# Optimization experiments

Hardware: AMD Instinct MI355X
Metric: run time of the kernel (lower is better)

## Reference

```python
import jax, jax.numpy as jnp
import numpy as np

N = 100000  # nodes
E = 1600000  # edges (before self-loops)
F_IN, F_HID, F_OUT = 64, 128, 64


def setup_inputs() -> dict:
    key = jax.random.key(0)
    ks = jax.random.split(key, 8)
    x = jax.random.normal(ks[0], (N, F_IN), dtype=jnp.float32)
    edge_index = jax.random.randint(ks[1], (2, E), 0, N, dtype=jnp.int64)
    # Glorot-ish init for weights, zero bias (PyG GCNConv default)
    W1 = jax.random.normal(ks[2], (F_IN, F_HID), dtype=jnp.float32) / np.sqrt(F_IN)
    W2 = jax.random.normal(ks[3], (F_HID, F_HID), dtype=jnp.float32) / np.sqrt(F_HID)
    W3 = jax.random.normal(ks[4], (F_HID, F_OUT), dtype=jnp.float32) / np.sqrt(F_HID)
    b1 = jnp.zeros((F_HID,), dtype=jnp.float32)
    b2 = jnp.zeros((F_HID,), dtype=jnp.float32)
    b3 = jnp.zeros((F_OUT,), dtype=jnp.float32)
    return {"x": x, "edge_index": edge_index, "W1": W1, "b1": b1,
            "W2": W2, "b2": b2, "W3": W3, "b3": b3}


def _gcn_norm(edge_index, num_nodes):
    """Add self-loops and compute symmetric D^-1/2 A D^-1/2 edge norms."""
    loop = jnp.arange(num_nodes, dtype=edge_index.dtype)
    src = jnp.concatenate([edge_index[0], loop])  # [E+N]
    dst = jnp.concatenate([edge_index[1], loop])  # [E+N]
    deg = jax.ops.segment_sum(jnp.ones_like(src, dtype=jnp.float32), dst,
                              num_segments=num_nodes)
    dinv = jnp.where(deg > 0, jax.lax.rsqrt(deg), 0.0)
    norm = dinv[src] * dinv[dst]  # [E+N]
    return src, dst, norm


def _gcn_conv(h, src, dst, norm, W, b, num_nodes):
    hw = h @ W                                   # [N, out] dense transform
    msg = hw[src] * norm[:, None]                # gather + edge scale
    out = jax.ops.segment_sum(msg, dst, num_segments=num_nodes)  # scatter-add
    return out + b


def reference(x, edge_index, W1, b1, W2, b2, W3, b3):
    src, dst, norm = _gcn_norm(edge_index, N)
    h = jax.nn.relu(_gcn_conv(x, src, dst, norm, W1, b1, N))
    h = jax.nn.relu(_gcn_conv(h, src, dst, norm, W2, b2, N))
    return _gcn_conv(h, src, dst, norm, W3, b3, N)
```

## Files before the change

kernel.cpp:

```cpp
#include <hip/hip_runtime.h>
#include <hip/hip_bf16.h>
#include <hip/hip_fp16.h>


typedef _Float16 h8 __attribute__((ext_vector_type(8)));
typedef float f4 __attribute__((ext_vector_type(4)));

constexpr int BSHIFT = 7;
constexpr int BNODES = 1 << BSHIFT;
constexpr int PB     = 256;
constexpr int CAP    = 4096;

__device__ inline void load8h(const _Float16* p, float* f) {
    h8 v = *(const h8*)p;
#pragma unroll
    for (int j = 0; j < 8; j++) f[j] = (float)v[j];
}

__device__ inline void store8h(_Float16* p, const float* f) {
    h8 v;
#pragma unroll
    for (int j = 0; j < 8; j++) v[j] = (_Float16)f[j];
    *(h8*)p = v;
}

__device__ inline void store4h(_Float16* p, float4 v) {
    _Float16 t[4] = {(_Float16)v.x, (_Float16)v.y, (_Float16)v.z, (_Float16)v.w};
    *(uint2*)p = *(uint2*)t;
}

__global__ __launch_bounds__(256) void phist_k(const int* __restrict__ dst,
                                               int* __restrict__ hist,
                                               int E, int nbuck, int chunk) {
    __shared__ int h[1024];
    for (int i = threadIdx.x; i < nbuck; i += 256) h[i] = 0;
    __syncthreads();
    int beg = blockIdx.x * chunk;
    int end = min(E, beg + chunk);
    for (int e = beg + threadIdx.x; e < end; e += 256)
        atomicAdd(&h[dst[e] >> BSHIFT], 1);
    __syncthreads();
    for (int i = threadIdx.x; i < nbuck; i += 256)
        hist[(long)blockIdx.x * nbuck + i] = h[i];
}

__global__ __launch_bounds__(256) void scan_blocks_k(const int* __restrict__ in,
                                                     int* __restrict__ excl,
                                                     int* __restrict__ bsums, int n) {
    __shared__ int s[256];
    int tid = threadIdx.x;
    int i = blockIdx.x * 256 + tid;
    int v = (i < n) ? in[i] : 0;
    s[tid] = v;
    __syncthreads();
    for (int off = 1; off < 256; off <<= 1) {
        int t = (tid >= off) ? s[tid - off] : 0;
        __syncthreads();
        s[tid] += t;
        __syncthreads();
    }
    if (i < n) excl[i] = s[tid] - v;
    if (tid == 255) bsums[blockIdx.x] = s[255];
}

__global__ __launch_bounds__(1024) void mid_k(int* __restrict__ bsums, int nb,
                                              const int* __restrict__ hist,
                                              int* __restrict__ bbase,
                                              int nbuck, int E) {
    __shared__ int s[1024];
    int tid = threadIdx.x;
    int v = 0;
    if (blockIdx.x == 0) {
        v = (tid < nb) ? bsums[tid] : 0;
    } else {
        if (tid < nbuck) {
            int t0 = 0, t1 = 0, t2 = 0, t3 = 0;
            for (int j = 0; j < PB; j += 4) {
                t0 += hist[(long)(j + 0) * nbuck + tid];
                t1 += hist[(long)(j + 1) * nbuck + tid];
                t2 += hist[(long)(j + 2) * nbuck + tid];
                t3 += hist[(long)(j + 3) * nbuck + tid];
            }
            v = (t0 + t1) + (t2 + t3);
        }
    }
    s[tid] = v;
    __syncthreads();
    for (int off = 1; off < 1024; off <<= 1) {
        int t = (tid >= off) ? s[tid - off] : 0;
        __syncthreads();
        s[tid] += t;
        __syncthreads();
    }
    if (blockIdx.x == 0) {
        if (tid < nb) bsums[tid] = s[tid] - v;
    } else {
        if (tid < nbuck) bbase[tid] = s[tid] - v;
        if (tid == 0) bbase[nbuck] = E;
    }
}

__global__ __launch_bounds__(256) void part2_k(const int* __restrict__ src,
                                               const int* __restrict__ dst,
                                               const int* __restrict__ offs,
                                               const int* __restrict__ bsums,
                                               unsigned* __restrict__ ebuf,
                                               int E, int nbuck, int chunk) {
    __shared__ int cur[1024];
    for (int i = threadIdx.x; i < nbuck; i += 256) {
        long flat = (long)blockIdx.x * nbuck + i;
        cur[i] = offs[flat] + bsums[flat >> 8];
    }
    __syncthreads();
    int beg = blockIdx.x * chunk;
    int end = min(E, beg + chunk);
    for (int e = beg + threadIdx.x; e < end; e += 256) {
        int d = dst[e];
        int b = d >> BSHIFT;
        int pos = atomicAdd(&cur[b], 1);
        ebuf[pos] = ((unsigned)(d & (BNODES - 1)) << 25) | (unsigned)src[e];
    }
}

__global__ __launch_bounds__(256) void finalize_k(const unsigned* __restrict__ ebuf,
                                                  const int* __restrict__ hist,
                                                  const int* __restrict__ offs,
                                                  const int* __restrict__ bsums,
                                                  const int* __restrict__ bbase,
                                                  int nbuck,
                                                  int* __restrict__ rowst,
                                                  int* __restrict__ rowend,
                                                  float* __restrict__ dinv,
                                                  int* __restrict__ col,
                                                  const float* __restrict__ x,
                                                  _Float16* __restrict__ msgX, int N) {
    __shared__ unsigned se[CAP];
    __shared__ int cj[PB], sj[PB], sb[PB];
    __shared__ int cnt_s[BNODES], scan_s[BNODES], cur_s[BNODES];
    __shared__ float di_s[BNODES];

    int b = blockIdx.x, tid = threadIdx.x;
    int node0 = b << BSHIFT;
    int nn = min(BNODES, N - node0);
    int beg = bbase[b];

    if (tid < PB) {
        long flat = (long)tid * nbuck + b;
        cj[tid] = hist[flat];
        sj[tid] = offs[flat] + bsums[flat >> 8];
    }
    if (tid < BNODES) cnt_s[tid] = 0;
    __syncthreads();

    if (tid < PB) sb[tid] = cj[tid];
    __syncthreads();
    for (int off = 1; off < PB; off <<= 1) {
        int t = 0;
        if (tid < PB && tid >= off) t = sb[tid - off];
        __syncthreads();
        if (tid < PB) sb[tid] += t;
        __syncthreads();
    }
    int m = sb[PB - 1];
    __syncthreads();

    {
        int j = tid;
        int base = sb[j] - cj[j], c = cj[j], s0 = sj[j];
        for (int k = 0; k < c; k++) {
            unsigned e = ebuf[s0 + k];
            int idx = base + k;
            if (idx < CAP) se[idx] = e;
            else atomicAdd(&cnt_s[e >> 25], 1);
        }
    }
    __syncthreads();

    int mcap = m < CAP ? m : CAP;
    for (int i = tid; i < mcap; i += 256) atomicAdd(&cnt_s[se[i] >> 25], 1);
    __syncthreads();

    int v = (tid < BNODES) ? cnt_s[tid] : 0;
    if (tid < BNODES) scan_s[tid] = v;
    __syncthreads();
    for (int off = 1; off < BNODES; off <<= 1) {
        int t = 0;
        if (tid < BNODES && tid >= off) t = scan_s[tid - off];
        __syncthreads();
        if (tid < BNODES) scan_s[tid] += t;
        __syncthreads();
    }
    if (tid < nn) {
        int ex = scan_s[tid] - v;
        int st = beg + ex;
        rowst[node0 + tid] = st;
        rowend[node0 + tid] = st + v;
        float di = rsqrtf((float)v + 1.0f);
        dinv[node0 + tid] = di;
        di_s[tid] = di;
        cur_s[tid] = ex;
    }
    __syncthreads();

    for (int i = tid; i < mcap; i += 256) {
        unsigned e = se[i];
        int p = atomicAdd(&cur_s[e >> 25], 1);
        col[beg + p] = (int)(e & 0x1FFFFFFu);
    }
    if (m > CAP) {
        int j = tid;
        int base = sb[j] - cj[j], c = cj[j], s0 = sj[j];
        for (int k = 0; k < c; k++) {
            int idx = base + k;
            if (idx >= CAP) {
                unsigned e = ebuf[s0 + k];
                int p = atomicAdd(&cur_s[e >> 25], 1);
                col[beg + p] = (int)(e & 0x1FFFFFFu);
            }
        }
    }

    for (int t = tid; t < nn * 16; t += 256) {
        int nl = t >> 4, q = t & 15;
        int node = node0 + nl;
        float4 vx = *(const float4*)(x + (long)node * 64 + q * 4);
        float di = di_s[nl];
        vx.x *= di; vx.y *= di; vx.z *= di; vx.w *= di;
        store4h(msgX + (long)node * 64 + q * 4, vx);
    }
}

template <int K, int FOUT, bool BIAS, bool RELU, bool DINV_OUT>
__global__ __launch_bounds__(256) void fag_k(const _Float16* __restrict__ msg,
                                             const int* __restrict__ rowst,
                                             const int* __restrict__ rowend,
                                             const int* __restrict__ col,
                                             const float* __restrict__ dinv,
                                             const _Float16* __restrict__ Wsw,
                                             const float* __restrict__ bias,
                                             _Float16* __restrict__ C, int n) {
    constexpr int NT = FOUT / 16, NC = K / 32;
    constexpr int LDK = K + 8;
    constexpr int LPN = K / 8;
    constexpr int NPB = 256 / LPN;
    __shared__ _Float16 As[64 * LDK];

    int tid = threadIdx.x;
    int row0 = blockIdx.x * 64;

#pragma unroll
    for (int pass = 0; pass < 64 / NPB; pass++) {
        int nl = pass * NPB + tid / LPN;
        int q = tid % LPN;
        int node = row0 + nl;
        float acc[8];
        if (node < n) {
            load8h(msg + (long)node * K + q * 8, acc);
            int beg = rowst[node], end = rowend[node];
            int e = beg;
            for (; e + 4 <= end; e += 4) {
                int s0 = col[e], s1 = col[e + 1], s2 = col[e + 2], s3 = col[e + 3];
                h8 v0 = *(const h8*)(msg + (long)s0 * K + q * 8);
                h8 v1 = *(const h8*)(msg + (long)s1 * K + q * 8);
                h8 v2 = *(const h8*)(msg + (long)s2 * K + q * 8);
                h8 v3 = *(const h8*)(msg + (long)s3 * K + q * 8);
#pragma unroll
                for (int j = 0; j < 8; j++)
                    acc[j] += ((float)v0[j] + (float)v1[j]) + ((float)v2[j] + (float)v3[j]);
            }
            for (; e < end; e++) {
                int s = col[e];
                h8 v = *(const h8*)(msg + (long)s * K + q * 8);
#pragma unroll
                for (int j = 0; j < 8; j++) acc[j] += (float)v[j];
            }
            float di = dinv[node];
#pragma unroll
            for (int j = 0; j < 8; j++) acc[j] *= di;
        } else {
#pragma unroll
            for (int j = 0; j < 8; j++) acc[j] = 0.f;
        }
        h8 o;
#pragma unroll
        for (int j = 0; j < 8; j++) o[j] = (_Float16)acc[j];
        *(h8*)(As + nl * LDK + q * 8) = o;
    }
    __syncthreads();

    int lane = tid & 63, wave = tid >> 6;
    int quad = lane >> 4, cl = lane & 15;
    int r0 = wave * 16;

    h8 a[NC];
#pragma unroll
    for (int c = 0; c < NC; c++)
        a[c] = *(const h8*)(As + (r0 + cl) * LDK + quad * 8 + c * 32);

    f4 acc2[NT];
#pragma unroll
    for (int t = 0; t < NT; t++) acc2[t] = (f4){0.f, 0.f, 0.f, 0.f};

    const h8* wv = (const h8*)Wsw;
#pragma unroll
    for (int c = 0; c < NC; c++) {
#pragma unroll
        for (int t = 0; t < NT; t++)
            acc2[t] = __builtin_amdgcn_mfma_f32_16x16x32_f16(
                a[c], wv[(c * NT + t) * 64 + lane], acc2[t], 0, 0, 0);
    }

#pragma unroll
    for (int t = 0; t < NT; t++) {
        int c0 = t * 16 + cl;
        float bb = BIAS ? bias[c0] : 0.f;
#pragma unroll
        for (int r = 0; r < 4; r++) {
            int row = row0 + r0 + quad * 4 + r;
            if (row >= n) continue;
            float v = acc2[t][r] + bb;
            if (RELU) v = fmaxf(v, 0.f);
            if (DINV_OUT) v *= dinv[row];
            C[(long)row * FOUT + c0] = (_Float16)v;
        }
    }
}

template <int F, bool BIAS, bool F16OUT>
__global__ __launch_bounds__(256) void agg_f16_k(const _Float16* __restrict__ msg,
                                                 const int* __restrict__ rowst,
                                                 const int* __restrict__ rowend,
                                                 const int* __restrict__ col,
                                                 const float* __restrict__ dinv,
                                                 const float* __restrict__ b,
                                                 void* __restrict__ out, int n) {
    constexpr int LPN = F / 8;
    constexpr int NPB = 256 / LPN;
    int node = blockIdx.x * NPB + threadIdx.x / LPN;
    int q = threadIdx.x % LPN;
    if (node >= n) return;

    float acc[8];
    load8h(msg + (long)node * F + q * 8, acc);

    int beg = rowst[node], end = rowend[node];
    int e = beg;
    for (; e + 8 <= end; e += 8) {
        h8 v[8];
#pragma unroll
        for (int u = 0; u < 8; u++)
            v[u] = *(const h8*)(msg + (long)col[e + u] * F + q * 8);
#pragma unroll
        for (int j = 0; j < 8; j++)
            acc[j] += (((float)v[0][j] + (float)v[1][j]) + ((float)v[2][j] + (float)v[3][j])) +
                      (((float)v[4][j] + (float)v[5][j]) + ((float)v[6][j] + (float)v[7][j]));
    }
    for (; e + 4 <= end; e += 4) {
        h8 v0 = *(const h8*)(msg + (long)col[e] * F + q * 8);
        h8 v1 = *(const h8*)(msg + (long)col[e + 1] * F + q * 8);
        h8 v2 = *(const h8*)(msg + (long)col[e + 2] * F + q * 8);
        h8 v3 = *(const h8*)(msg + (long)col[e + 3] * F + q * 8);
#pragma unroll
        for (int j = 0; j < 8; j++)
            acc[j] += ((float)v0[j] + (float)v1[j]) + ((float)v2[j] + (float)v3[j]);
    }
    for (; e < end; e++) {
        h8 v = *(const h8*)(msg + (long)col[e] * F + q * 8);
#pragma unroll
        for (int j = 0; j < 8; j++) acc[j] += (float)v[j];
    }

    float di = dinv[node];
    float o[8];
#pragma unroll
    for (int j = 0; j < 8; j++) o[j] = di * acc[j];
    if (BIAS) {
#pragma unroll
        for (int j = 0; j < 8; j++) o[j] += b[q * 8 + j];
    }
    if (F16OUT) {
        store8h((_Float16*)out + (long)node * F + q * 8, o);
    } else {
        float* dst = (float*)out + (long)node * F + q * 8;
        *(float4*)dst = make_float4(o[0], o[1], o[2], o[3]);
        *(float4*)(dst + 4) = make_float4(o[4], o[5], o[6], o[7]);
    }
}

template <int K, int FOUT>
__device__ inline void wfrag(const float* __restrict__ W,
                             _Float16* __restrict__ Wsw, int t) {
    constexpr int NT = FOUT / 16;
    int lane = t & 63;
    int tile = (t >> 6) % NT;
    int chunk = (t >> 6) / NT;
    int kbase = chunk * 32 + (lane >> 4) * 8;
    int nc = tile * 16 + (lane & 15);
    h8 v;
#pragma unroll
    for (int j = 0; j < 8; j++) v[j] = (_Float16)W[(kbase + j) * FOUT + nc];
    ((h8*)Wsw)[t] = v;
}

__global__ __launch_bounds__(256) void wprep3_k(const float* __restrict__ W1,
                                                const float* __restrict__ W2,
                                                const float* __restrict__ W3,
                                                _Float16* __restrict__ w1s,
                                                _Float16* __restrict__ w2s,
                                                _Float16* __restrict__ w3s) {
    int t = blockIdx.x * 256 + threadIdx.x;
    if (t < 1024) wfrag<64, 128>(W1, w1s, t);
    else if (t < 3072) wfrag<128, 128>(W2, w2s, t - 1024);
    else if (t < 4096) wfrag<128, 64>(W3, w3s, t - 3072);
}

__global__ __launch_bounds__(256) void dgemm_k(const _Float16* __restrict__ A,
                                               const _Float16* __restrict__ w2s,
                                               const _Float16* __restrict__ w3s,
                                               const float* __restrict__ b2,
                                               const float* __restrict__ dinv,
                                               _Float16* __restrict__ C, int n) {
    constexpr int LDK = 136;
    __shared__ _Float16 Hs[64 * LDK];

    int tid = threadIdx.x, lane = tid & 63, wave = tid >> 6;
    int quad = lane >> 4, cl = lane & 15;
    int row0 = blockIdx.x * 64, r0 = wave * 16;

    h8 a[4];
    const _Float16* arow = A + (long)(row0 + r0 + cl) * 128 + quad * 8;
#pragma unroll
    for (int c = 0; c < 4; c++) a[c] = *(const h8*)(arow + c * 32);

    f4 acc1[8];
#pragma unroll
    for (int t = 0; t < 8; t++) acc1[t] = (f4){0.f, 0.f, 0.f, 0.f};
    const h8* wv2 = (const h8*)w2s;
#pragma unroll
    for (int c = 0; c < 4; c++) {
#pragma unroll
        for (int t = 0; t < 8; t++)
            acc1[t] = __builtin_amdgcn_mfma_f32_16x16x32_f16(
                a[c], wv2[(c * 8 + t) * 64 + lane], acc1[t], 0, 0, 0);
    }

#pragma unroll
    for (int t = 0; t < 8; t++) {
        int c0 = t * 16 + cl;
        float bb = b2[c0];
#pragma unroll
        for (int r = 0; r < 4; r++) {
            float v = fmaxf(acc1[t][r] + bb, 0.f);
            Hs[(r0 + quad * 4 + r) * LDK + c0] = (_Float16)v;
        }
    }
    __builtin_amdgcn_s_waitcnt(0);

    h8 a2[4];
#pragma unroll
    for (int c = 0; c < 4; c++)
        a2[c] = *(const h8*)(Hs + (r0 + cl) * LDK + quad * 8 + c * 32);

    f4 acc2[4];
#pragma unroll
    for (int t = 0; t < 4; t++) acc2[t] = (f4){0.f, 0.f, 0.f, 0.f};
    const h8* wv3 = (const h8*)w3s;
#pragma unroll
    for (int c = 0; c < 4; c++) {
#pragma unroll
        for (int t = 0; t < 4; t++)
            acc2[t] = __builtin_amdgcn_mfma_f32_16x16x32_f16(
                a2[c], wv3[(c * 4 + t) * 64 + lane], acc2[t], 0, 0, 0);
    }

#pragma unroll
    for (int t = 0; t < 4; t++) {
        int c0 = t * 16 + cl;
#pragma unroll
        for (int r = 0; r < 4; r++) {
            int row = row0 + r0 + quad * 4 + r;
            if (row >= n) continue;
            float v = acc2[t][r] * dinv[row];
            C[(long)row * 64 + c0] = (_Float16)v;
        }
    }
}

extern "C" void kernel_launch(void* const* d_in, const int* in_sizes, int n_in,
                              void* d_out, int out_size, void* d_ws, size_t ws_size,
                              hipStream_t stream) {
    const float* x  = (const float*)d_in[0];
    const int*   ei = (const int*)d_in[1];
    const float* W1 = (const float*)d_in[2];
    const float* b1 = (const float*)d_in[3];
    const float* W2 = (const float*)d_in[4];
    const float* b2 = (const float*)d_in[5];
    const float* W3 = (const float*)d_in[6];
    const float* b3 = (const float*)d_in[7];
    float* out = (float*)d_out;

    const int N = in_sizes[0] / 64;
    const int E = in_sizes[1] / 2;
    const int* src = ei;
    const int* dst = ei + E;
    const int nbuck = (N + BNODES - 1) >> BSHIFT;
    const int chunk = (E + PB - 1) / PB;
    const int n2 = PB * nbuck;
    const int nb2 = (n2 + 255) / 256;

    int*   hist   = (int*)d_ws;
    int*   offs   = hist + n2;
    int*   bsums  = offs + n2;
    int*   bbase  = bsums + 1024;
    int*   rowst  = bbase + nbuck + 1;
    int*   rowend = rowst + N;
    float* dinv   = (float*)(rowend + N);
    int*   col    = (int*)(dinv + N);
    _Float16* w1s = (_Float16*)(col + E);
    _Float16* w2s = w1s + 64 * 128;
    _Float16* w3s = w2s + 128 * 128;
    float* P      = (float*)(w3s + 128 * 64);
    float* Q      = P + (long)N * 128;

    _Float16* msgX  = (_Float16*)P;
    unsigned* ebuf  = (unsigned*)Q;
    _Float16* msg1  = (_Float16*)Q;
    _Float16* aggH1 = (_Float16*)P;
    _Float16* msg3  = (_Float16*)Q;

    const int gb = (N + 63) / 64;

    wprep3_k<<<16, 256, 0, stream>>>(W1, W2, W3, w1s, w2s, w3s);

    phist_k<<<PB, 256, 0, stream>>>(dst, hist, E, nbuck, chunk);
    scan_blocks_k<<<nb2, 256, 0, stream>>>(hist, offs, bsums, n2);
    mid_k<<<2, 1024, 0, stream>>>(bsums, nb2, hist, bbase, nbuck, E);
    part2_k<<<PB, 256, 0, stream>>>(src, dst, offs, bsums, ebuf, E, nbuck, chunk);
    finalize_k<<<nbuck, 256, 0, stream>>>(ebuf, hist, offs, bsums, bbase, nbuck,
                                          rowst, rowend, dinv, col, x, msgX, N);

    fag_k<64, 128, true, true, true><<<gb, 256, 0, stream>>>(
        msgX, rowst, rowend, col, dinv, w1s, b1, msg1, N);

    agg_f16_k<128, false, true><<<(N + 15) / 16, 256, 0, stream>>>(
        msg1, rowst, rowend, col, dinv, nullptr, (void*)aggH1, N);

    dgemm_k<<<gb, 256, 0, stream>>>(aggH1, w2s, w3s, b2, dinv, msg3, N);

    agg_f16_k<64, true, false><<<(N + 31) / 32, 256, 0, stream>>>(
        msg3, rowst, rowend, col, dinv, b3, (void*)out, N);
}
```

Measured before the change: 383.6 us.

## Split aggregation kernels into feature slices for cache locality

The CSR aggregation kernels are changed so each block handles only one of eight feature slices (16 halfs for F=128, 8 halfs for F=64), with blockIdx low bits selecting the slice. Each gathered row segment is therefore narrower, so more rows of a slice fit in L2/MALL, which is meant to raise cache hit rates on the random neighbor gathers. In exchange, col indices and row pointers are re-read once per slice, and each gather becomes a 16-byte access per row, giving less coalescing per lane.

```diff
diff --git a/kernel.cpp b/kernel.cpp
--- a/kernel.cpp
+++ b/kernel.cpp
@@ -326,22 +326,26 @@
     }
 }
 
-template <int F, bool BIAS, bool F16OUT>
-__global__ __launch_bounds__(256) void agg_f16_k(const _Float16* __restrict__ msg,
-                                                 const int* __restrict__ rowst,
-                                                 const int* __restrict__ rowend,
-                                                 const int* __restrict__ col,
-                                                 const float* __restrict__ dinv,
-                                                 const float* __restrict__ b,
-                                                 void* __restrict__ out, int n) {
-    constexpr int LPN = F / 8;
-    constexpr int NPB = 256 / LPN;
-    int node = blockIdx.x * NPB + threadIdx.x / LPN;
-    int q = threadIdx.x % LPN;
+template <int F, int FS, bool BIAS, bool F16OUT>
+__global__ __launch_bounds__(256) void agg_slice_k(const _Float16* __restrict__ msg,
+                                                   const int* __restrict__ rowst,
+                                                   const int* __restrict__ rowend,
+                                                   const int* __restrict__ col,
+                                                   const float* __restrict__ dinv,
+                                                   const float* __restrict__ b,
+                                                   void* __restrict__ out, int n) {
+    constexpr int LPS = FS / 8;
+    constexpr int NPB = 256 / LPS;
+    int slice = blockIdx.x & 7;
+    int blk   = blockIdx.x >> 3;
+    int node  = blk * NPB + threadIdx.x / LPS;
+    int q     = threadIdx.x % LPS;
     if (node >= n) return;
+    int f0 = slice * FS + q * 8;
+    const _Float16* mp = msg + f0;
 
     float acc[8];
-    load8h(msg + (long)node * F + q * 8, acc);
+    load8h(mp + (long)node * F, acc);
 
     int beg = rowst[node], end = rowend[node];
     int e = beg;
@@ -349,23 +353,23 @@
         h8 v[8];
 #pragma unroll
         for (int u = 0; u < 8; u++)
-            v[u] = *(const h8*)(msg + (long)col[e + u] * F + q * 8);
+            v[u] = *(const h8*)(mp + (long)col[e + u] * F);
 #pragma unroll
         for (int j = 0; j < 8; j++)
             acc[j] += (((float)v[0][j] + (float)v[1][j]) + ((float)v[2][j] + (float)v[3][j])) +
                       (((float)v[4][j] + (float)v[5][j]) + ((float)v[6][j] + (float)v[7][j]));
     }
     for (; e + 4 <= end; e += 4) {
-        h8 v0 = *(const h8*)(msg + (long)col[e] * F + q * 8);
-        h8 v1 = *(const h8*)(msg + (long)col[e + 1] * F + q * 8);
-        h8 v2 = *(const h8*)(msg + (long)col[e + 2] * F + q * 8);
-        h8 v3 = *(const h8*)(msg + (long)col[e + 3] * F + q * 8);
+        h8 v0 = *(const h8*)(mp + (long)col[e] * F);
+        h8 v1 = *(const h8*)(mp + (long)col[e + 1] * F);
+        h8 v2 = *(const h8*)(mp + (long)col[e + 2] * F);
+        h8 v3 = *(const h8*)(mp + (long)col[e + 3] * F);
 #pragma unroll
         for (int j = 0; j < 8; j++)
             acc[j] += ((float)v0[j] + (float)v1[j]) + ((float)v2[j] + (float)v3[j]);
     }
     for (; e < end; e++) {
-        h8 v = *(const h8*)(msg + (long)col[e] * F + q * 8);
+        h8 v = *(const h8*)(mp + (long)col[e] * F);
 #pragma unroll
         for (int j = 0; j < 8; j++) acc[j] += (float)v[j];
     }
@@ -376,14 +380,14 @@
     for (int j = 0; j < 8; j++) o[j] = di * acc[j];
     if (BIAS) {
 #pragma unroll
-        for (int j = 0; j < 8; j++) o[j] += b[q * 8 + j];
+        for (int j = 0; j < 8; j++) o[j] += b[f0 + j];
     }
     if (F16OUT) {
-        store8h((_Float16*)out + (long)node * F + q * 8, o);
+        store8h((_Float16*)out + (long)node * F + f0, o);
     } else {
-        float* dst = (float*)out + (long)node * F + q * 8;
-        *(float4*)dst = make_float4(o[0], o[1], o[2], o[3]);
-        *(float4*)(dst + 4) = make_float4(o[4], o[5], o[6], o[7]);
+        float* d = (float*)out + (long)node * F + f0;
+        *(float4*)d = make_float4(o[0], o[1], o[2], o[3]);
+        *(float4*)(d + 4) = make_float4(o[4], o[5], o[6], o[7]);
     }
 }
 
@@ -542,11 +546,13 @@
     fag_k<64, 128, true, true, true><<<gb, 256, 0, stream>>>(
         msgX, rowst, rowend, col, dinv, w1s, b1, msg1, N);
 
-    agg_f16_k<128, false, true><<<(N + 15) / 16, 256, 0, stream>>>(
+    const int nb128 = (N + 127) / 128;
+    agg_slice_k<128, 16, false, true><<<8 * nb128, 256, 0, stream>>>(
         msg1, rowst, rowend, col, dinv, nullptr, (void*)aggH1, N);
 
     dgemm_k<<<gb, 256, 0, stream>>>(aggH1, w2s, w3s, b2, dinv, msg3, N);
 
-    agg_f16_k<64, true, false><<<(N + 31) / 32, 256, 0, stream>>>(
+    const int nb256 = (N + 255) / 256;
+    agg_slice_k<64, 8, true, false><<<8 * nb256, 256, 0, stream>>>(
         msg3, rowst, rowend, col, dinv, b3, (void*)out, N);
 }
```

Result: slower. 913.2 us (+138.1%).

## Slice layer-2 features into 16-column planes for cache-local aggregation

Applied to the files above, without the earlier changes.

The first fused aggregate-GEMM now writes its 128-wide output as eight 16-column slices, each stored contiguously over all nodes. A new aggregation kernel processes one slice per block, so the random gathers for a slice touch a working set of about 3.2 MB that can stay in cache. Each node's edges are split across four lanes and combined with shuffles. The following GEMM reads its A operand from this sliced layout. The cost is that every edge list is read eight times and the gathers are smaller (16 bytes each), in exchange for better cache hit rates.

```diff
diff --git a/kernel.cpp b/kernel.cpp
--- a/kernel.cpp
+++ b/kernel.cpp
@@ -230,7 +230,7 @@
     }
 }
 
-template <int K, int FOUT, bool BIAS, bool RELU, bool DINV_OUT>
+template <int K, int FOUT, bool BIAS, bool RELU, bool DINV_OUT, bool SMOUT>
 __global__ __launch_bounds__(256) void fag_k(const _Float16* __restrict__ msg,
                                              const int* __restrict__ rowst,
                                              const int* __restrict__ rowend,
@@ -321,8 +321,68 @@
             float v = acc2[t][r] + bb;
             if (RELU) v = fmaxf(v, 0.f);
             if (DINV_OUT) v *= dinv[row];
-            C[(long)row * FOUT + c0] = (_Float16)v;
+            if (SMOUT)
+                C[((long)t * n + row) * 16 + cl] = (_Float16)v;
+            else
+                C[(long)row * FOUT + c0] = (_Float16)v;
         }
+    }
+}
+
+__global__ __launch_bounds__(256) void agg_ep2_k(const _Float16* __restrict__ msg,
+                                                 const int* __restrict__ rowst,
+                                                 const int* __restrict__ rowend,
+                                                 const int* __restrict__ col,
+                                                 const float* __restrict__ dinv,
+                                                 _Float16* __restrict__ out, int n) {
+    int slice = blockIdx.x & 7;
+    int blk   = blockIdx.x >> 3;
+    int tid   = threadIdx.x;
+    int node  = blk * 32 + (tid >> 3);
+    int eslot = (tid >> 1) & 3;
+    int q     = tid & 1;
+    if (node >= n) return;
+    const _Float16* mp = msg + (long)slice * n * 16 + q * 8;
+
+    float acc[8];
+    if (eslot == 0) {
+        load8h(mp + (long)node * 16, acc);
+    } else {
+#pragma unroll
+        for (int j = 0; j < 8; j++) acc[j] = 0.f;
+    }
+
+    int beg = rowst[node], end = rowend[node];
+    int e = beg + eslot;
+    for (; e + 12 < end; e += 16) {
+        int s0 = col[e], s1 = col[e + 4], s2 = col[e + 8], s3 = col[e + 12];
+        h8 v0 = *(const h8*)(mp + (long)s0 * 16);
+        h8 v1 = *(const h8*)(mp + (long)s1 * 16);
+        h8 v2 = *(const h8*)(mp + (long)s2 * 16);
+        h8 v3 = *(const h8*)(mp + (long)s3 * 16);
+#pragma unroll
+        for (int j = 0; j < 8; j++)
+            acc[j] += (((float)v0[j] + (float)v1[j]) + ((float)v2[j] + (float)v3[j]));
+    }
+    for (; e < end; e += 4) {
+        int s = col[e];
+        h8 v = *(const h8*)(mp + (long)s * 16);
+#pragma unroll
+        for (int j = 0; j < 8; j++) acc[j] += (float)v[j];
+    }
+
+#pragma unroll
+    for (int j = 0; j < 8; j++) {
+        acc[j] += __shfl_xor(acc[j], 2);
+        acc[j] += __shfl_xor(acc[j], 4);
+    }
+
+    if ((tid & 6) == 0) {
+        float di = dinv[node];
+        float o[8];
+#pragma unroll
+        for (int j = 0; j < 8; j++) o[j] = di * acc[j];
+        store8h(out + ((long)slice * n + node) * 16 + q * 8, o);
     }
 }
 
@@ -426,11 +486,14 @@
     int tid = threadIdx.x, lane = tid & 63, wave = tid >> 6;
     int quad = lane >> 4, cl = lane & 15;
     int row0 = blockIdx.x * 64, r0 = wave * 16;
+    int arow = row0 + r0 + cl;
 
     h8 a[4];
-    const _Float16* arow = A + (long)(row0 + r0 + cl) * 128 + quad * 8;
-#pragma unroll
-    for (int c = 0; c < 4; c++) a[c] = *(const h8*)(arow + c * 32);
+#pragma unroll
+    for (int c = 0; c < 4; c++) {
+        int sl = c * 2 + (quad >> 1);
+        a[c] = *(const h8*)(A + ((long)sl * n + arow) * 16 + (quad & 1) * 8);
+    }
 
     f4 acc1[8];
 #pragma unroll
@@ -525,7 +588,7 @@
     _Float16* msgX  = (_Float16*)P;
     unsigned* ebuf  = (unsigned*)Q;
     _Float16* msg1  = (_Float16*)Q;
-    _Float16* aggH1 = (_Float16*)P;
+    _Float16* aggH2 = (_Float16*)P;
     _Float16* msg3  = (_Float16*)Q;
 
     const int gb = (N + 63) / 64;
@@ -539,13 +602,14 @@
     finalize_k<<<nbuck, 256, 0, stream>>>(ebuf, hist, offs, bsums, bbase, nbuck,
                                           rowst, rowend, dinv, col, x, msgX, N);
 
-    fag_k<64, 128, true, true, true><<<gb, 256, 0, stream>>>(
+    fag_k<64, 128, true, true, true, true><<<gb, 256, 0, stream>>>(
         msgX, rowst, rowend, col, dinv, w1s, b1, msg1, N);
 
-    agg_f16_k<128, false, true><<<(N + 15) / 16, 256, 0, stream>>>(
-        msg1, rowst, rowend, col, dinv, nullptr, (void*)aggH1, N);
-
-    dgemm_k<<<gb, 256, 0, stream>>>(aggH1, w2s, w3s, b2, dinv, msg3, N);
+    const int nb32 = (N + 31) / 32;
+    agg_ep2_k<<<8 * nb32, 256, 0, stream>>>(
+        msg1, rowst, rowend, col, dinv, aggH2, N);
+
+    dgemm_k<<<gb, 256, 0, stream>>>(aggH2, w2s, w3s, b2, dinv, msg3, N);
 
     agg_f16_k<64, true, false><<<(N + 31) / 32, 256, 0, stream>>>(
         msg3, rowst, rowend, col, dinv, b3, (void*)out, N);
```

New measurement: 384.6 us. Within noise of the previous version (+0.2%).
